# Kernel optimization log

Hardware: AMD Instinct MI355X
Metric: run time of the kernel (lower is better)

## Reference

```python
import jax, jax.numpy as jnp
import numpy as np

V, D, H, L, RATIO, T_MAX = 1024, 512, 8, 11, 3, 1024
DH = D // H
HID = D * RATIO
NB, DB = 2048, 128  # bigram buckets / dim
EPS = 1e-6


def _rope_tables(T):
    pos = jnp.arange(T, dtype=jnp.float32)
    freqs = 1.0 / (10000.0 ** (jnp.arange(0, DH, 2, dtype=jnp.float32) / DH))
    emb = jnp.outer(pos, freqs)  # [T, DH/2]
    return jnp.cos(emb), jnp.sin(emb)


def _rmsnorm(x, w):
    return x * jax.lax.rsqrt(jnp.mean(x * x, axis=-1, keepdims=True) + EPS) * w


def setup_inputs() -> dict:
    key = jax.random.key(0)
    ks = jax.random.split(key, 10)
    B, T = 8, 1024
    s = 0.02
    return {
        "x": jax.random.randint(ks[0], (B, T), 0, V),
        "embed": jax.random.normal(ks[1], (V, D), jnp.float32) * s,
        "Wqkv": jax.random.normal(ks[2], (L, 3 * D, D), jnp.float32) * s,
        "Wproj": jax.random.normal(ks[3], (L, D, D), jnp.float32) * s,
        "n1_w": jnp.ones((L, D), jnp.float32),
        "n2_w": jnp.ones((L, D), jnp.float32),
        "Wfc1": jax.random.normal(ks[4], (L, HID, D), jnp.float32) * s,
        "Wfc2": jax.random.normal(ks[5], (L, D, HID), jnp.float32) * s,
        "norm_f_w": jnp.ones((D,), jnp.float32),
        "bg_embed": jax.random.normal(ks[6], (NB, DB), jnp.float32) * s,
        "bg_proj": jax.random.normal(ks[7], (V, DB), jnp.float32) * s,
    }


def _attn(x, Wqkv, Wproj, cos, sin, causal):
    B, T, C = x.shape
    qkv = x @ Wqkv.T  # [B,T,3D]
    q, k, v = jnp.split(qkv, 3, axis=-1)
    def heads(t):
        return t.reshape(B, T, H, DH).transpose(0, 2, 1, 3)  # [B,H,T,DH]
    q, k, v = heads(q), heads(k), heads(v)
    c = cos[None, None]  # [1,1,T,DH/2]
    s = sin[None, None]
    def rope(t):
        t1, t2 = t[..., : DH // 2], t[..., DH // 2 :]
        return jnp.concatenate([t1 * c - t2 * s, t1 * s + t2 * c], axis=-1)
    q, k = rope(q), rope(k)
    w = jnp.einsum("bhqd,bhkd->bhqk", q, k) * (DH ** -0.5)
    w = jnp.where(causal, w, -jnp.inf)
    w = jax.nn.softmax(w.astype(jnp.float32), axis=-1).astype(x.dtype)
    out = jnp.einsum("bhqk,bhkd->bhqd", w, v)
    self_w = jnp.diagonal(w, axis1=-2, axis2=-1)[..., None]  # [B,H,T,1]
    out = out - self_w * v  # XSA: subtract self-value contribution
    out = out.transpose(0, 2, 1, 3).reshape(B, T, C)
    return out @ Wproj.T


def reference(x, embed, Wqkv, Wproj, n1_w, n2_w, Wfc1, Wfc2, norm_f_w, bg_embed, bg_proj):
    B, T = x.shape
    cos, sin = _rope_tables(T_MAX)
    cos, sin = cos[:T], sin[:T]
    causal = jnp.tril(jnp.ones((T, T), dtype=bool))
    # bigram logits from previous token
    prev = jnp.concatenate([jnp.zeros((B, 1), x.dtype), x[:, :-1]], axis=1)
    bigram_logits = bg_embed[prev % NB] @ bg_proj.T  # [B,T,V]
    h = embed[x]
    for i in range(L):
        h = h + _attn(_rmsnorm(h, n1_w[i]), Wqkv[i], Wproj[i], cos, sin, causal)
        z = _rmsnorm(h, n2_w[i])
        h = h + jnp.square(jax.nn.relu(z @ Wfc1[i].T)) @ Wfc2[i].T
    h = _rmsnorm(h, norm_f_w)
    return h @ embed.T + bigram_logits
```

## Files before the change

kernel.cpp:

```cpp
#include <hip/hip_runtime.h>

#define NROW   8192
#define DMODEL 512
#define TSEQ   1024
#define LAYERS 11
#define HIDDEN 1536

typedef __bf16 bf16_t;
typedef bf16_t bf16x8 __attribute__((ext_vector_type(8)));
typedef bf16_t bf16x4 __attribute__((ext_vector_type(4)));
typedef float  f32x4  __attribute__((ext_vector_type(4)));
typedef unsigned int u32;
typedef u32 u32x4 __attribute__((ext_vector_type(4)));

#define GLD16(gp, lp) __builtin_amdgcn_global_load_lds( \
    (const __attribute__((address_space(1))) void*)(gp), \
    (__attribute__((address_space(3))) void*)(lp), 16, 0, 0)

#if __has_builtin(__builtin_amdgcn_exp2f)
#define EXP2(x) __builtin_amdgcn_exp2f(x)
#else
#define EXP2(x) exp2f(x)
#endif

__global__ void rope_table_k(float* __restrict__ cosT, float* __restrict__ sinT) {
    int i = blockIdx.x * blockDim.x + threadIdx.x;
    int t = i >> 5, j = i & 31;
    float freq = powf(10000.f, -(float)j * (1.f / 32.f));
    float ang = (float)t * freq;
    cosT[i] = cosf(ang);
    sinT[i] = sinf(ang);
}

__global__ void embed_gather_k(const int* __restrict__ x,
                               const float* __restrict__ embed,
                               float* __restrict__ h,
                               bf16_t* __restrict__ hb) {
    int n = blockIdx.x;
    int d = threadIdx.x;
    float4 v = ((const float4*)(embed + (size_t)x[n] * DMODEL))[d];
    ((float4*)(h + (size_t)n * DMODEL))[d] = v;
    bf16x4 o;
    o[0] = (bf16_t)v.x; o[1] = (bf16_t)v.y; o[2] = (bf16_t)v.z; o[3] = (bf16_t)v.w;
    *(bf16x4*)(hb + (size_t)n * DMODEL + d * 4) = o;
}

__global__ void bg_gather_k(const int* __restrict__ x,
                            const float* __restrict__ bge,
                            bf16_t* __restrict__ Afu) {
    int n = blockIdx.x;
    int t = n & (TSEQ - 1);
    int prev = (t == 0) ? 0 : x[n - 1];
    Afu[(size_t)n * 640 + 512 + threadIdx.x] = (bf16_t)bge[(size_t)prev * 128 + threadIdx.x];
}

__global__ void cvt_bf16_k(const float* __restrict__ in, bf16_t* __restrict__ out, int n8) {
    int i = blockIdx.x * blockDim.x + threadIdx.x;
    if (i >= n8) return;
    float4 a = ((const float4*)in)[2 * i];
    float4 b = ((const float4*)in)[2 * i + 1];
    bf16x8 o;
    o[0] = (bf16_t)a.x; o[1] = (bf16_t)a.y; o[2] = (bf16_t)a.z; o[3] = (bf16_t)a.w;
    o[4] = (bf16_t)b.x; o[5] = (bf16_t)b.y; o[6] = (bf16_t)b.z; o[7] = (bf16_t)b.w;
    ((bf16x8*)out)[i] = o;
}

__global__ void cvt_fold_k(const float* __restrict__ in,
                           const float* __restrict__ nw,
                           bf16_t* __restrict__ out, int n8, int layerSz) {
    int i = blockIdx.x * blockDim.x + threadIdx.x;
    if (i >= n8) return;
    int i8 = i * 8;
    int k = i8 & 511;
    int l = i8 / layerSz;
    const float* wv = nw + l * DMODEL + k;
    float4 a = ((const float4*)in)[2 * i];
    float4 b = ((const float4*)in)[2 * i + 1];
    float4 wa = *(const float4*)wv;
    float4 wb = *(const float4*)(wv + 4);
    bf16x8 o;
    o[0] = (bf16_t)(a.x * wa.x); o[1] = (bf16_t)(a.y * wa.y);
    o[2] = (bf16_t)(a.z * wa.z); o[3] = (bf16_t)(a.w * wa.w);
    o[4] = (bf16_t)(b.x * wb.x); o[5] = (bf16_t)(b.y * wb.y);
    o[6] = (bf16_t)(b.z * wb.z); o[7] = (bf16_t)(b.w * wb.w);
    ((bf16x8*)out)[i] = o;
}

__global__ void cvt_pad_k(const float* __restrict__ in, bf16_t* __restrict__ out,
                          int n8, int lshift, int mask, int colOff) {
    int i = blockIdx.x * blockDim.x + threadIdx.x;
    if (i >= n8) return;
    int i8 = i * 8;
    int row = i8 >> lshift;
    int col = i8 & mask;
    float4 a = ((const float4*)in)[2 * i];
    float4 b = ((const float4*)in)[2 * i + 1];
    bf16x8 o;
    o[0] = (bf16_t)a.x; o[1] = (bf16_t)a.y; o[2] = (bf16_t)a.z; o[3] = (bf16_t)a.w;
    o[4] = (bf16_t)b.x; o[5] = (bf16_t)b.y; o[6] = (bf16_t)b.z; o[7] = (bf16_t)b.w;
    *(bf16x8*)&out[(size_t)row * 640 + colOff + col] = o;
}

__global__ __launch_bounds__(256) void scale_k(const bf16_t* __restrict__ hb,
                                               float* __restrict__ s) {
    int wv = threadIdx.x >> 6, lane = threadIdx.x & 63;
    int row = (blockIdx.x << 2) + wv;
    bf16x8 v = *(const bf16x8*)(hb + (size_t)row * DMODEL + lane * 8);
    float ss = 0.f;
#pragma unroll
    for (int j = 0; j < 8; ++j) { float f = (float)v[j]; ss += f * f; }
#pragma unroll
    for (int off = 32; off; off >>= 1) ss += __shfl_xor(ss, off, 64);
    if (lane == 0) s[row] = rsqrtf(ss * (1.f / DMODEL) + 1e-6f);
}

__global__ __launch_bounds__(256) void rmsnorm_k(const float* __restrict__ in,
                                                 const float* __restrict__ w,
                                                 bf16_t* __restrict__ out,
                                                 int ostride) {
    int wv = threadIdx.x >> 6, lane = threadIdx.x & 63;
    int row = (blockIdx.x << 2) + wv;
    const float* rp = in + (size_t)row * DMODEL + lane * 8;
    float4 v0 = *(const float4*)(rp);
    float4 v1 = *(const float4*)(rp + 4);
    float ss = v0.x*v0.x + v0.y*v0.y + v0.z*v0.z + v0.w*v0.w
             + v1.x*v1.x + v1.y*v1.y + v1.z*v1.z + v1.w*v1.w;
#pragma unroll
    for (int off = 32; off; off >>= 1) ss += __shfl_xor(ss, off, 64);
    float sc = rsqrtf(ss * (1.f / DMODEL) + 1e-6f);
    const float* wp = w + lane * 8;
    float4 w0 = *(const float4*)(wp);
    float4 w1 = *(const float4*)(wp + 4);
    bf16x8 o;
    o[0] = (bf16_t)(v0.x * sc * w0.x); o[1] = (bf16_t)(v0.y * sc * w0.y);
    o[2] = (bf16_t)(v0.z * sc * w0.z); o[3] = (bf16_t)(v0.w * sc * w0.w);
    o[4] = (bf16_t)(v1.x * sc * w1.x); o[5] = (bf16_t)(v1.y * sc * w1.y);
    o[6] = (bf16_t)(v1.z * sc * w1.z); o[7] = (bf16_t)(v1.w * sc * w1.w);
    *(bf16x8*)(out + (size_t)row * ostride + lane * 8) = o;
}

template<int BM, int EPI>
__global__ __launch_bounds__(256, 2)
void gemm_mfma(const bf16_t* __restrict__ A,
               const bf16_t* __restrict__ B,
               float* __restrict__ Cf,
               bf16_t* __restrict__ Cb,
               const float* __restrict__ cosT,
               const float* __restrict__ sinT,
               const float* __restrict__ Sc,
               int M, int N, int K, int nbx) {
    constexpr int NT  = 256;
    constexpr int WM  = 2;
    constexpr int MI  = BM / WM / 16;
    constexpr int ACH = (BM * 4) / NT;
    constexpr int BCH = 2;
    constexpr int NBUF = (BM == 64) ? 4 : 3;
    constexpr bool SCALED = (EPI == 2 || EPI == 4);
    __shared__ __align__(16) bf16_t As[NBUF][BM * 32];
    __shared__ __align__(16) bf16_t Bs[NBUF][128 * 32];
    const int tid = threadIdx.x;
    const int w = tid >> 6, lane = tid & 63;

    const int nwg = (int)gridDim.x;
    const int bid = blockIdx.x;
    const int swz = (bid & 7) * (nwg >> 3) + (bid >> 3);
    const int bx = swz % nbx, by = swz / nbx;

    const int m0 = by * BM, n0 = bx * 128;
    const int wr = (w >> 1) * (BM / WM), wc = (w & 1) * 64;
    const int fr = lane & 15, fq = lane >> 4;

    f32x4 acc[MI][4] = {};

    float sld[SCALED ? MI : 1][4];
    if constexpr (SCALED) {
#pragma unroll
        for (int i = 0; i < MI; ++i)
#pragma unroll
            for (int q = 0; q < 4; ++q)
                sld[i][q] = Sc[m0 + wr + i * 16 + fq * 4 + q];
    }
    float cold[EPI == 1 ? MI : 1][4][4];
    if constexpr (EPI == 1) {
#pragma unroll
        for (int i = 0; i < MI; ++i)
#pragma unroll
            for (int j = 0; j < 4; ++j)
#pragma unroll
                for (int q = 0; q < 4; ++q)
                    cold[i][j][q] = Cf[(size_t)(m0 + wr + i * 16 + fq * 4 + q) * N
                                       + n0 + wc + j * 16 + fr];
    }

    auto stage = [&](int k0, int buf) {
#pragma unroll
        for (int c = 0; c < ACH; ++c) {
            int idx = c * NT + tid;
            int row = idx >> 2, cs = idx & 3;
            GLD16(A + (size_t)(m0 + row) * K + k0 + cs * 8,
                  &As[buf][(size_t)(c * NT + w * 64) * 8]);
        }
#pragma unroll
        for (int c = 0; c < BCH; ++c) {
            int idx = c * NT + tid;
            int row = idx >> 2, cs = idx & 3;
            GLD16(B + (size_t)(n0 + row) * K + k0 + cs * 8,
                  &Bs[buf][(size_t)(c * NT + w * 64) * 8]);
        }
    };

    const int NK = K >> 5;
    stage(0, 0);
    stage(32, 1);
    for (int k = 0; k < NK; ++k) {
        const int cur = k % NBUF;
        if (k + 2 < NK) {
            stage((k + 2) << 5, (k + 2) % NBUF);
            if constexpr (BM == 128) asm volatile("s_waitcnt vmcnt(8)" ::: "memory");
            else                     asm volatile("s_waitcnt vmcnt(6)" ::: "memory");
        } else if (k + 1 < NK) {
            if constexpr (BM == 128) asm volatile("s_waitcnt vmcnt(4)" ::: "memory");
            else                     asm volatile("s_waitcnt vmcnt(3)" ::: "memory");
        } else {
            asm volatile("s_waitcnt vmcnt(0)" ::: "memory");
        }
        __builtin_amdgcn_s_barrier();
        __builtin_amdgcn_sched_barrier(0);

        bf16x8 a[MI], b[4];
        const bf16_t* ap = &As[cur][(size_t)(wr + fr) * 32 + fq * 8];
        const bf16_t* bp = &Bs[cur][(size_t)(wc + fr) * 32 + fq * 8];
#pragma unroll
        for (int i = 0; i < MI; ++i) a[i] = *(const bf16x8*)(ap + i * 16 * 32);
#pragma unroll
        for (int j = 0; j < 4; ++j)  b[j] = *(const bf16x8*)(bp + j * 16 * 32);
        __builtin_amdgcn_s_setprio(1);
#pragma unroll
        for (int i = 0; i < MI; ++i)
#pragma unroll
            for (int j = 0; j < 4; ++j)
                acc[i][j] = __builtin_amdgcn_mfma_f32_16x16x32_bf16(a[i], b[j], acc[i][j], 0, 0, 0);
        __builtin_amdgcn_s_setprio(0);

        if constexpr (NBUF == 3) {
            asm volatile("s_waitcnt lgkmcnt(0)" ::: "memory");
            __builtin_amdgcn_s_barrier();
            __builtin_amdgcn_sched_barrier(0);
        }
    }

    if (EPI == 4) {
        const bool qk = (n0 + wc) < 1024;
#pragma unroll
        for (int i = 0; i < MI; ++i) {
#pragma unroll
            for (int q = 0; q < 4; ++q) {
                int row = m0 + wr + i * 16 + fq * 4 + q;
                size_t rb = (size_t)row * N + n0 + wc;
                float sm = sld[i][q];
                if (qk) {
                    int t = row & (TSEQ - 1);
#pragma unroll
                    for (int j = 0; j < 2; ++j) {
                        int d = j * 16 + fr;
                        float c = cosT[t * 32 + d];
                        float s = sinT[t * 32 + d];
                        float v1 = acc[i][j][q] * sm, v2 = acc[i][j + 2][q] * sm;
                        Cb[rb + j * 16 + fr]       = (bf16_t)(v1 * c - v2 * s);
                        Cb[rb + (j + 2) * 16 + fr] = (bf16_t)(v1 * s + v2 * c);
                    }
                } else {
#pragma unroll
                    for (int j = 0; j < 4; ++j)
                        Cb[rb + j * 16 + fr] = (bf16_t)(acc[i][j][q] * sm);
                }
            }
        }
        return;
    }
#pragma unroll
    for (int i = 0; i < MI; ++i) {
        int row = m0 + wr + i * 16 + fq * 4;
#pragma unroll
        for (int j = 0; j < 4; ++j) {
            int col = n0 + wc + j * 16 + fr;
#pragma unroll
            for (int q = 0; q < 4; ++q) {
                float v = acc[i][j][q];
                size_t off = (size_t)(row + q) * N + col;
                if (EPI == 0)      Cf[off] = v;
                else if (EPI == 1) {
                    float nv = cold[i][j][q] + v;
                    Cf[off] = nv;
                    Cb[off] = (bf16_t)nv;
                } else if (EPI == 2) {
                    v = fmaxf(v * sld[i][q], 0.f);
                    Cb[off] = (bf16_t)(v * v);
                }
            }
        }
    }
}

__global__ __launch_bounds__(512) void attn_mfma_k(const bf16_t* __restrict__ qkvb,
                                                   bf16_t* __restrict__ outb) {
    __shared__ __align__(16) bf16_t Ks[2][64 * 64];
    __shared__ __align__(16) bf16_t VsT[2][2 * 64 * 32];

    const int tid = threadIdx.x;
    const int w  = tid >> 6;
    const int ln = tid & 63;
    const int lr = ln & 15;
    const int lg = ln >> 4;

    const int bid = blockIdx.x;
    const int p  = 7 - (bid >> 6);
    const int bh = bid & 63;
    const int b = bh >> 3, h = bh & 7;
    const int lastT = (p << 7) + 64;
    const int tq0  = (p << 7) + w * 16;
    const int qrow = tq0 + lr;
    const int wlast = tq0 & ~63;

    const bf16_t* Qg = qkvb + (size_t)b * TSEQ * 1536 + h * 64;
    const bf16_t* Kg = Qg + 512;
    const bf16_t* Vg = Qg + 1024;

    const int mk = tid >> 4;
    const int md = tid & 15;
    const int src0 = lr + 32 * (lg & 1);
    const int fsel = lg >> 1;
    const int gofs = 8 * (lg ^ ((lr >> 2) & 3));

    auto KSTAGE = [&](int t0, int buf) {
        int key = w * 8 + (ln >> 3);
        int dc  = (ln & 7) ^ (ln >> 3);
        GLD16(Kg + (size_t)(t0 + key) * 1536 + dc * 8, &Ks[buf][w * 512]);
    };
    auto VLOAD = [&](int t0, bf16x4* rv) {
#pragma unroll
        for (int i = 0; i < 4; ++i)
            rv[i] = *(const bf16x4*)(Vg + (size_t)(t0 + mk * 4 + i) * 1536 + md * 4);
    };
    auto VWRITE = [&](const bf16x4* rv, int buf) {
        const int s = mk >> 3;
#pragma unroll
        for (int j = 0; j < 4; ++j) {
            int row = md * 4 + j;
            bf16x4 wv;
            wv[0] = rv[0][j]; wv[1] = rv[1][j]; wv[2] = rv[2][j]; wv[3] = rv[3][j];
            int g = (mk & 7) ^ ((md & 3) << 1);
            *(bf16x4*)&VsT[buf][s * 2048 + row * 32 + g * 4] = wv;
        }
    };

    bf16x8 qreg[2];
    {
        const float QS = 0.1803368801f;
        const bf16_t* qp = Qg + (size_t)qrow * 1536 + lg * 8;
        qreg[0] = *(const bf16x8*)qp;
        qreg[1] = *(const bf16x8*)(qp + 32);
#pragma unroll
        for (int j = 0; j < 8; ++j) {
            qreg[0][j] = (bf16_t)((float)qreg[0][j] * QS);
            qreg[1][j] = (bf16_t)((float)qreg[1][j] * QS);
        }
    }

    f32x4 accO[4] = {};
    float mrun = -1e30f, pl = 0.f, esf = 0.f;

    {
        bf16x4 rv[4];
        KSTAGE(0, 0);
        if (w < 4) VLOAD(0, rv);
        asm volatile("s_waitcnt vmcnt(0)" ::: "memory");
        if (w < 4) VWRITE(rv, 0);
        asm volatile("s_waitcnt lgkmcnt(0)" ::: "memory");
        __builtin_amdgcn_s_barrier();
        __builtin_amdgcn_sched_barrier(0);
    }

    for (int t0 = 0; t0 <= lastT; t0 += 64) {
        const int cur = (t0 >> 6) & 1;
        const bool more = t0 < lastT;
        bf16x4 rv[4];
        if (more) {
            KSTAGE(t0 + 64, cur ^ 1);
            if (w < 4) VLOAD(t0 + 64, rv);
        }

        if (t0 <= wlast) {
            const bool masked = t0 == wlast;

            f32x4 sq[4] = {};
            __builtin_amdgcn_s_setprio(1);
#pragma unroll
            for (int kr = 0; kr < 4; ++kr) {
                int key = kr * 16 + lr;
#pragma unroll
                for (int s = 0; s < 2; ++s) {
                    int chunk = key * 8 + ((s * 4 + lg) ^ (key & 7));
                    bf16x8 kf = *(const bf16x8*)&Ks[cur][chunk * 8];
                    sq[kr] = __builtin_amdgcn_mfma_f32_16x16x32_bf16(kf, qreg[s], sq[kr], 0, 0, 0);
                }
            }
            __builtin_amdgcn_s_setprio(0);

            float e16[4][4];
            float tm = -1e30f;
            if (masked) {
#pragma unroll
                for (int f = 0; f < 4; ++f)
#pragma unroll
                    for (int r = 0; r < 4; ++r) {
                        int key = t0 + f * 16 + lg * 4 + r;
                        float sv = (key <= qrow) ? sq[f][r] : -1e30f;
                        e16[f][r] = sv;
                        tm = fmaxf(tm, sv);
                    }
            } else {
#pragma unroll
                for (int f = 0; f < 4; ++f)
#pragma unroll
                    for (int r = 0; r < 4; ++r) {
                        e16[f][r] = sq[f][r];
                        tm = fmaxf(tm, sq[f][r]);
                    }
            }
            tm = fmaxf(tm, __shfl_xor(tm, 16, 64));
            tm = fmaxf(tm, __shfl_xor(tm, 32, 64));

            const bool resc = __any(tm > mrun + 8.f);
            float mnew = resc ? fmaxf(mrun, tm) : mrun;
            float psum = 0.f;
#pragma unroll
            for (int f = 0; f < 4; ++f)
#pragma unroll
                for (int r = 0; r < 4; ++r) {
                    float e = EXP2(e16[f][r] - mnew);
                    e16[f][r] = e;
                    psum += e;
                }
            float pd = 0.f;
            if (masked) {
#pragma unroll
                for (int f = 0; f < 4; ++f)
#pragma unroll
                    for (int r = 0; r < 4; ++r) {
                        int key = t0 + f * 16 + lg * 4 + r;
                        pd = (key == qrow) ? e16[f][r] : pd;
                    }
            }
            if (resc) {
                float corr = EXP2(mrun - mnew);
                mrun = mnew;
                pl  = pl  * corr + psum;
                esf = esf * corr + pd;
#pragma unroll
                for (int dblk = 0; dblk < 4; ++dblk)
#pragma unroll
                    for (int r = 0; r < 4; ++r) accO[dblk][r] *= corr;
            } else {
                pl  += psum;
                esf += pd;
            }

            u32 plo[4], phi[4];
#pragma unroll
            for (int f = 0; f < 4; ++f) {
                bf16x4 t;
                t[0] = (bf16_t)e16[f][0]; t[1] = (bf16_t)e16[f][1];
                t[2] = (bf16_t)e16[f][2]; t[3] = (bf16_t)e16[f][3];
                uint2 pr = __builtin_bit_cast(uint2, t);
                plo[f] = pr.x; phi[f] = pr.y;
            }

#pragma unroll
            for (int s = 0; s < 2; ++s) {
                u32 a0 = (u32)__shfl((int)plo[s * 2],     src0,      64);
                u32 a1 = (u32)__shfl((int)phi[s * 2],     src0,      64);
                u32 a2 = (u32)__shfl((int)plo[s * 2],     src0 + 16, 64);
                u32 a3 = (u32)__shfl((int)phi[s * 2],     src0 + 16, 64);
                u32 c0 = (u32)__shfl((int)plo[s * 2 + 1], src0,      64);
                u32 c1 = (u32)__shfl((int)phi[s * 2 + 1], src0,      64);
                u32 c2 = (u32)__shfl((int)plo[s * 2 + 1], src0 + 16, 64);
                u32 c3 = (u32)__shfl((int)phi[s * 2 + 1], src0 + 16, 64);
                u32x4 bw;
                bw[0] = fsel ? c0 : a0;
                bw[1] = fsel ? c1 : a1;
                bw[2] = fsel ? c2 : a2;
                bw[3] = fsel ? c3 : a3;
                bf16x8 bfrag = __builtin_bit_cast(bf16x8, bw);
                __builtin_amdgcn_s_setprio(1);
#pragma unroll
                for (int dblk = 0; dblk < 4; ++dblk) {
                    bf16x8 av = *(const bf16x8*)&VsT[cur][s * 2048 + (dblk * 16 + lr) * 32 + gofs];
                    accO[dblk] = __builtin_amdgcn_mfma_f32_16x16x32_bf16(av, bfrag, accO[dblk], 0, 0, 0);
                }
                __builtin_amdgcn_s_setprio(0);
            }
        }

        if (more) {
            asm volatile("s_waitcnt vmcnt(0)" ::: "memory");
            if (w < 4) VWRITE(rv, cur ^ 1);
            asm volatile("s_waitcnt lgkmcnt(0)" ::: "memory");
            __builtin_amdgcn_s_barrier();
            __builtin_amdgcn_sched_barrier(0);
        }
    }

    pl  += __shfl_xor(pl, 16, 64);  pl  += __shfl_xor(pl, 32, 64);
    esf += __shfl_xor(esf, 16, 64); esf += __shfl_xor(esf, 32, 64);
    float rin = 1.0f / pl;
    const bf16_t* vqp = Vg + (size_t)qrow * 1536;
    bf16_t* op = outb + (size_t)(b * TSEQ + qrow) * DMODEL + h * 64;
#pragma unroll
    for (int dblk = 0; dblk < 4; ++dblk) {
        bf16x4 vq = *(const bf16x4*)(vqp + dblk * 16 + lg * 4);
        bf16x4 o4;
#pragma unroll
        for (int r = 0; r < 4; ++r)
            o4[r] = (bf16_t)((accO[dblk][r] - esf * (float)vq[r]) * rin);
        *(bf16x4*)(op + dblk * 16 + lg * 4) = o4;
    }
}

static inline void cvt(const float* in, bf16_t* out, size_t n, hipStream_t s) {
    int n8 = (int)(n / 8);
    cvt_bf16_k<<<(n8 + 255) / 256, 256, 0, s>>>(in, out, n8);
}

extern "C" void kernel_launch(void* const* d_in, const int* in_sizes, int n_in,
                              void* d_out, int out_size, void* d_ws, size_t ws_size,
                              hipStream_t stream) {
    const int*   x     = (const int*)d_in[0];
    const float* embed = (const float*)d_in[1];
    const float* Wqkv  = (const float*)d_in[2];
    const float* Wproj = (const float*)d_in[3];
    const float* n1w   = (const float*)d_in[4];
    const float* n2w   = (const float*)d_in[5];
    const float* Wfc1  = (const float*)d_in[6];
    const float* Wfc2  = (const float*)d_in[7];
    const float* normf = (const float*)d_in[8];
    const float* bge   = (const float*)d_in[9];
    const float* bgp   = (const float*)d_in[10];
    float* out = (float*)d_out;

    float* ws   = (float*)d_ws;
    float* cosT = ws;
    float* sinT = cosT + 32768;
    float* h    = sinT + 32768;
    bf16_t* qkvb = (bf16_t*)(h + (size_t)NROW * DMODEL);
    bf16_t* ub   = qkvb;
    bf16_t* Afu  = qkvb;
    bf16_t* hb   = qkvb + (size_t)NROW * 1536;
    bf16_t* atb  = hb  + (size_t)NROW * DMODEL;
    bf16_t* wqb  = atb + (size_t)NROW * DMODEL;
    bf16_t* wpb  = wqb + (size_t)LAYERS * 3 * DMODEL * DMODEL;
    bf16_t* w1b  = wpb + (size_t)LAYERS * DMODEL * DMODEL;
    bf16_t* w2b  = w1b + (size_t)LAYERS * HIDDEN * DMODEL;
    bf16_t* bfu  = w2b + (size_t)LAYERS * DMODEL * HIDDEN;
    float*  sbuf = (float*)(bfu + (size_t)1024 * 640);

    rope_table_k<<<128, 256, 0, stream>>>(cosT, sinT);
    embed_gather_k<<<NROW, 128, 0, stream>>>(x, embed, h, hb);

    {
        int n8q = (int)((size_t)LAYERS * 3 * DMODEL * DMODEL / 8);
        cvt_fold_k<<<(n8q + 255) / 256, 256, 0, stream>>>(Wqkv, n1w, wqb, n8q, 3 * DMODEL * DMODEL);
        int n81 = (int)((size_t)LAYERS * HIDDEN * DMODEL / 8);
        cvt_fold_k<<<(n81 + 255) / 256, 256, 0, stream>>>(Wfc1, n2w, w1b, n81, HIDDEN * DMODEL);
    }
    cvt(Wproj, wpb, (size_t)LAYERS * DMODEL * DMODEL, stream);
    cvt(Wfc2,  w2b, (size_t)LAYERS * DMODEL * HIDDEN, stream);
    cvt_pad_k<<<(65536 + 255) / 256, 256, 0, stream>>>(embed, bfu, 65536, 9, 511, 0);
    cvt_pad_k<<<(16384 + 255) / 256, 256, 0, stream>>>(bgp,   bfu, 16384, 7, 127, 512);

    for (int i = 0; i < LAYERS; ++i) {
        scale_k<<<NROW / 4, 256, 0, stream>>>(hb, sbuf);
        gemm_mfma<128, 4><<<768, 256, 0, stream>>>(
            hb, wqb + (size_t)i * 3 * DMODEL * DMODEL, nullptr, qkvb,
            cosT, sinT, sbuf, NROW, 3 * DMODEL, DMODEL, 12);
        attn_mfma_k<<<512, 512, 0, stream>>>(qkvb, atb);
        gemm_mfma<64, 1><<<512, 256, 0, stream>>>(
            atb, wpb + (size_t)i * DMODEL * DMODEL, h, hb,
            nullptr, nullptr, nullptr, NROW, DMODEL, DMODEL, 4);
        scale_k<<<NROW / 4, 256, 0, stream>>>(hb, sbuf);
        gemm_mfma<128, 2><<<768, 256, 0, stream>>>(
            hb, w1b + (size_t)i * HIDDEN * DMODEL, nullptr, ub,
            nullptr, nullptr, sbuf, NROW, HIDDEN, DMODEL, 12);
        gemm_mfma<64, 1><<<512, 256, 0, stream>>>(
            ub, w2b + (size_t)i * DMODEL * HIDDEN, h, hb,
            nullptr, nullptr, nullptr, NROW, DMODEL, HIDDEN, 4);
    }

    rmsnorm_k<<<NROW / 4, 256, 0, stream>>>(h, normf, Afu, 640);
    bg_gather_k<<<NROW, 128, 0, stream>>>(x, bge, Afu);
    gemm_mfma<128, 0><<<512, 256, 0, stream>>>(
        Afu, bfu, out, nullptr, nullptr, nullptr, nullptr, NROW, 1024, 640, 8);
}
```

Baseline: 1.444 ms.

## Use one barrier per k-step in GEMM and XCD-aware attention block mapping

```diff
diff --git a/kernel.cpp b/kernel.cpp
--- a/kernel.cpp
+++ b/kernel.cpp
@@ -154,10 +154,9 @@
     constexpr int MI  = BM / WM / 16;
     constexpr int ACH = (BM * 4) / NT;
     constexpr int BCH = 2;
-    constexpr int NBUF = (BM == 64) ? 4 : 3;
     constexpr bool SCALED = (EPI == 2 || EPI == 4);
-    __shared__ __align__(16) bf16_t As[NBUF][BM * 32];
-    __shared__ __align__(16) bf16_t Bs[NBUF][128 * 32];
+    __shared__ __align__(16) bf16_t As[3][BM * 32];
+    __shared__ __align__(16) bf16_t Bs[3][128 * 32];
     const int tid = threadIdx.x;
     const int w = tid >> 6, lane = tid & 63;
 
@@ -213,9 +212,11 @@
     stage(0, 0);
     stage(32, 1);
     for (int k = 0; k < NK; ++k) {
-        const int cur = k % NBUF;
+        const int cur = k % 3;
+        __builtin_amdgcn_s_barrier();
+        __builtin_amdgcn_sched_barrier(0);
         if (k + 2 < NK) {
-            stage((k + 2) << 5, (k + 2) % NBUF);
+            stage((k + 2) << 5, (k + 2) % 3);
             if constexpr (BM == 128) asm volatile("s_waitcnt vmcnt(8)" ::: "memory");
             else                     asm volatile("s_waitcnt vmcnt(6)" ::: "memory");
         } else if (k + 1 < NK) {
@@ -224,7 +225,6 @@
         } else {
             asm volatile("s_waitcnt vmcnt(0)" ::: "memory");
         }
-        __builtin_amdgcn_s_barrier();
         __builtin_amdgcn_sched_barrier(0);
 
         bf16x8 a[MI], b[4];
@@ -241,12 +241,6 @@
             for (int j = 0; j < 4; ++j)
                 acc[i][j] = __builtin_amdgcn_mfma_f32_16x16x32_bf16(a[i], b[j], acc[i][j], 0, 0, 0);
         __builtin_amdgcn_s_setprio(0);
-
-        if constexpr (NBUF == 3) {
-            asm volatile("s_waitcnt lgkmcnt(0)" ::: "memory");
-            __builtin_amdgcn_s_barrier();
-            __builtin_amdgcn_sched_barrier(0);
-        }
     }
 
     if (EPI == 4) {
@@ -314,8 +308,12 @@
     const int lg = ln >> 4;
 
     const int bid = blockIdx.x;
-    const int p  = 7 - (bid >> 6);
-    const int bh = bid & 63;
+    const int xcd = bid & 7;
+    const int j   = bid >> 3;
+    const int mloc = j & 31;
+    const int g   = mloc >> 3;
+    const int p   = (j < 32) ? (7 - g) : g;
+    const int bh  = ((mloc & 7) << 3) | xcd;
     const int b = bh >> 3, h = bh & 7;
     const int lastT = (p << 7) + 64;
     const int tq0  = (p << 7) + w * 16;
@@ -345,12 +343,12 @@
     auto VWRITE = [&](const bf16x4* rv, int buf) {
         const int s = mk >> 3;
 #pragma unroll
-        for (int j = 0; j < 4; ++j) {
-            int row = md * 4 + j;
+        for (int jj = 0; jj < 4; ++jj) {
+            int row = md * 4 + jj;
             bf16x4 wv;
-            wv[0] = rv[0][j]; wv[1] = rv[1][j]; wv[2] = rv[2][j]; wv[3] = rv[3][j];
-            int g = (mk & 7) ^ ((md & 3) << 1);
-            *(bf16x4*)&VsT[buf][s * 2048 + row * 32 + g * 4] = wv;
+            wv[0] = rv[0][jj]; wv[1] = rv[1][jj]; wv[2] = rv[2][jj]; wv[3] = rv[3][jj];
+            int gx = (mk & 7) ^ ((md & 3) << 1);
+            *(bf16x4*)&VsT[buf][s * 2048 + row * 32 + gx * 4] = wv;
         }
     };
 
@@ -361,9 +359,9 @@
         qreg[0] = *(const bf16x8*)qp;
         qreg[1] = *(const bf16x8*)(qp + 32);
 #pragma unroll
-        for (int j = 0; j < 8; ++j) {
-            qreg[0][j] = (bf16_t)((float)qreg[0][j] * QS);
-            qreg[1][j] = (bf16_t)((float)qreg[1][j] * QS);
+        for (int jj = 0; jj < 8; ++jj) {
+            qreg[0][jj] = (bf16_t)((float)qreg[0][jj] * QS);
+            qreg[1][jj] = (bf16_t)((float)qreg[1][jj] * QS);
         }
     }
 
```

After: 1.471 ms. Within noise of the previous version (+1.9%).
